# Kernel optimization log

Hardware: AMD Instinct MI355X
Metric: run time of the kernel (lower is better)

## Reference

```python
import jax, jax.numpy as jnp
import numpy as np

G = 4          # conv groups (hardcoded in module)
C = 1024       # channels (hardcoded cin=cout=1024)
SCALE = 1.0 / np.sqrt(1024.0).astype(np.float32)  # 1/sqrt(c/h), h=1


def grouped_proj(x, W, b):
    # pointwise grouped Conv1d == block-diagonal matmul over channel groups
    # x: [B, C, P], W: [G, C//G out, C//G in], b: [C]
    B, C_, P = x.shape
    xg = x.reshape(B, G, C_ // G, P)
    y = jnp.einsum('goi,bgip->bgop', W, xg)  # [B, G, C//G, P]
    return y.reshape(B, C_, P) + b[None, :, None]


def setup_inputs() -> dict:
    key = jax.random.key(0)
    ks = jax.random.split(key, 8)
    B, PK, PQ = 8, 1024, 4096
    cg = C // G
    w_std = 1.0 / np.sqrt(cg).astype(np.float32)  # ~ conv default init scale
    return {
        'Xq': jax.random.normal(ks[0], (B, C, PQ), jnp.float32),
        'Xk': jax.random.normal(ks[1], (B, C, PK), jnp.float32),
        'Wq': jax.random.normal(ks[2], (G, cg, cg), jnp.float32) * w_std,
        'bq': jax.random.normal(ks[3], (C,), jnp.float32) * 0.01,
        'Wk': jax.random.normal(ks[4], (G, cg, cg), jnp.float32) * w_std,
        'bk': jax.random.normal(ks[5], (C,), jnp.float32) * 0.01,
        'Wv': jax.random.normal(ks[6], (G, cg, cg), jnp.float32) * w_std,
        'bv': jax.random.normal(ks[7], (C,), jnp.float32) * 0.01,
    }


def reference(Xq, Xk, Wq, bq, Wk, bk, Wv, bv):
    # Q and K are both projected from Xk; V from Xq (as in the torch code)
    Q = grouped_proj(Xk, Wq, bq)   # [B, C, Pk]
    K = grouped_proj(Xk, Wk, bk)   # [B, C, Pk]
    V = grouped_proj(Xq, Wv, bv)   # [B, C, Pq]
    b, c, pk = K.shape
    pq = V.shape[-1]
    h = 1
    Qh = Q.reshape(b, h, c // h, pk)
    Kh = K.reshape(b, h, c // h, pk)
    Vh = V.reshape(b, h, c // h, pq)
    # H: [B, h, Pk, Pq], contraction over channels; softmax over dim=-2 (Pk)
    H = jnp.einsum('bhci,bhcj->bhij', Kh, Vh) * SCALE
    H = jax.nn.softmax(H, axis=-2)
    # sparse_constrain: Gram over last axis vs identity, mean squared error
    mid = jnp.einsum('bhci,bhki->bhck', H, H)          # [B, h, Pk, Pk]
    Iden = jnp.eye(pk, dtype=H.dtype)[None, None]       # broadcast over B, h
    sparse_loss = jnp.mean((mid - Iden) ** 2)
    # out: mix Q along Pk with attention H -> [B, h, C, Pq]
    out = jnp.einsum('bhij,bhki->bhkj', H, Qh).reshape(b, c, pq)
    return out, sparse_loss, H
```

## Files before the change

kernel.cpp:

```cpp
#include <hip/hip_runtime.h>

typedef _Float16 f16;
typedef f16 f16x4 __attribute__((ext_vector_type(4)));
typedef f16 f16x8 __attribute__((ext_vector_type(8)));
typedef float f32x4 __attribute__((ext_vector_type(4)));

__device__ __forceinline__ void gload16(const void* g, void* ldsbase) {
  __builtin_amdgcn_global_load_lds((const __attribute__((address_space(1))) unsigned int*)g,
                                   (__attribute__((address_space(3))) unsigned int*)ldsbase, 16, 0, 0);
}

__device__ __forceinline__ int swz(int row, int c) {
  return row * 64 + ((c ^ ((row >> 1) & 3)) << 4);
}

template<int MODE>
__global__ void __launch_bounds__(512, 2)
gemm256(const f16* __restrict__ A, const f16* __restrict__ Bm, float* __restrict__ Cf,
        f16* __restrict__ E16, f16* __restrict__ E16t,
        int K, long sA, long sB, float scale, float* __restrict__ aux) {
  __shared__ f16 sb[65536];
  const int t = threadIdx.x, l = t & 63, w = t >> 6;
  const int wr = w >> 2, wc = w & 3;
  const int bid = blockIdx.x;
  const int swzb = (bid & 7) * 64 + (bid >> 3);
  const long b = swzb >> 6;
  const int inner = swzb & 63;
  const int bx = inner >> 2, by = inner & 3;
  const char* Abyte = (const char*)(A + b * sA + (long)(by * 256) * K);
  const char* Bbyte = (const char*)(Bm + b * sB + (long)(bx * 256) * K);

  int offSrc[4];
#pragma unroll
  for (int i = 0; i < 4; ++i) {
    int cid = i * 512 + t, row = cid >> 3, slot = cid & 7;
    offSrc[i] = row * (K * 2) + ((slot ^ (row & 7)) << 4);
  }
  int offAf[8][2], offBf[4][2];
#pragma unroll
  for (int mi = 0; mi < 8; ++mi) {
    int r = wr * 128 + mi * 16 + (l & 15);
#pragma unroll
    for (int ks = 0; ks < 2; ++ks)
      offAf[mi][ks] = r * 64 + ((((ks << 2) + (l >> 4)) ^ (r & 7)) << 3);
  }
#pragma unroll
  for (int ni = 0; ni < 4; ++ni) {
    int r = wc * 64 + ni * 16 + (l & 15);
#pragma unroll
    for (int ks = 0; ks < 2; ++ks)
      offBf[ni][ks] = r * 64 + ((((ks << 2) + (l >> 4)) ^ (r & 7)) << 3);
  }

  const int NT = K >> 6;
  f32x4 acc[8][4] = {};

  auto STAGE = [&](int kt, int bsel) {
    f16* la = sb + bsel * 32768;
    f16* lb = la + 16384;
    const char* as = Abyte + (long)kt * 128;
    const char* bs = Bbyte + (long)kt * 128;
#pragma unroll
    for (int i = 0; i < 4; ++i)
      gload16(as + offSrc[i], la + (i * 512 + (w << 6)) * 8);
#pragma unroll
    for (int i = 0; i < 4; ++i)
      gload16(bs + offSrc[i], lb + (i * 512 + (w << 6)) * 8);
  };

  STAGE(0, 0);
  for (int kt = 0; kt < NT; ++kt) {
    const int cur = kt & 1;
    if (kt + 1 < NT) {
      STAGE(kt + 1, cur ^ 1);
      asm volatile("s_waitcnt vmcnt(8)" ::: "memory");
    } else {
      asm volatile("s_waitcnt vmcnt(0)" ::: "memory");
    }
    __builtin_amdgcn_s_barrier();
    asm volatile("" ::: "memory");
    const f16* la = sb + cur * 32768;
    const f16* lb = la + 16384;
#pragma unroll
    for (int ks = 0; ks < 2; ++ks) {
      f16x8 bf[4];
#pragma unroll
      for (int ni = 0; ni < 4; ++ni) bf[ni] = *(const f16x8*)(lb + offBf[ni][ks]);
#pragma unroll
      for (int mi = 0; mi < 8; ++mi) {
        f16x8 af = *(const f16x8*)(la + offAf[mi][ks]);
#pragma unroll
        for (int ni = 0; ni < 4; ++ni)
          acc[mi][ni] = __builtin_amdgcn_mfma_f32_16x16x32_f16(af, bf[ni], acc[mi][ni], 0, 0, 0);
      }
    }
    asm volatile("s_waitcnt lgkmcnt(0)" ::: "memory");
    __builtin_amdgcn_s_barrier();
    asm volatile("" ::: "memory");
  }

  const int i0 = by * 256, j0 = bx * 256;
  if (MODE == 2) {
    float csum[4] = {};
#pragma unroll
    for (int mi = 0; mi < 8; ++mi)
#pragma unroll
      for (int ni = 0; ni < 4; ++ni)
#pragma unroll
        for (int q = 0; q < 4; ++q) {
          float e = __expf(acc[mi][ni][q] * scale);
          acc[mi][ni][q] = e;
          csum[ni] += e;
        }
#pragma unroll
    for (int ni = 0; ni < 4; ++ni) {
      csum[ni] += __shfl_xor(csum[ni], 16);
      csum[ni] += __shfl_xor(csum[ni], 32);
    }
    float* colp = (float*)(sb + 34816);
    if (l < 16) {
#pragma unroll
      for (int ni = 0; ni < 4; ++ni) colp[wr * 256 + wc * 64 + ni * 16 + l] = csum[ni];
    }
    __syncthreads();
    if (t < 256) aux[(b * 4 + by) * 4096 + bx * 256 + t] = colp[t] + colp[256 + t];
    f16* E16b = E16 + b * 4194304L;
    f16* E16tb = E16t + b * 4194304L;
#pragma unroll
    for (int s = 0; s < 4; ++s) {
      if (wr == (s >> 1)) {
        const int h = s & 1;
#pragma unroll
        for (int m2 = 0; m2 < 4; ++m2)
#pragma unroll
          for (int ni = 0; ni < 4; ++ni)
#pragma unroll
            for (int q = 0; q < 4; ++q)
              sb[(m2 * 16 + (l >> 4) * 4 + q) * 264 + wc * 64 + ni * 16 + (l & 15)] =
                  (f16)acc[h * 4 + m2][ni][q];
      }
      __syncthreads();
#pragma unroll
      for (int ii = 0; ii < 4; ++ii) {
        int cid = ii * 512 + t, r = cid >> 5, cc = cid & 31;
        *(f16x8*)(E16b + (long)(i0 + s * 64 + r) * 4096 + j0 + cc * 8) =
            *(const f16x8*)(sb + r * 264 + cc * 8);
      }
      const int q4 = w >> 1, r8 = l >> 3, ic = l & 7;
#pragma unroll
      for (int ii = 0; ii < 4; ++ii) {
        int j = q4 * 64 + r8 * 8 + (w & 1) * 4 + ii;
        f16x8 v;
#pragma unroll
        for (int k2 = 0; k2 < 8; ++k2) v[k2] = sb[(ic * 8 + k2) * 264 + j];
        *(f16x8*)(E16tb + (long)(j0 + j) * 1024 + i0 + s * 64 + ic * 8) = v;
      }
      __syncthreads();
    }
  }
}

__global__ void __launch_bounds__(512, 2)
fused3(const f16* __restrict__ Q, const f16* __restrict__ Et, float* __restrict__ Cf,
       const float* __restrict__ invg,
       const f16* __restrict__ E, const f16* __restrict__ inv2sg,
       float* __restrict__ Hf, float* __restrict__ midS) {
  __shared__ f16 sb[69632];
  const int t = threadIdx.x, l = t & 63, w = t >> 6;
  const int wr = w >> 2, wc = w & 3;

  if (blockIdx.x < 160) {
    const int bid = blockIdx.x;
    const long b = bid & 7;
    const int rest = bid >> 3;
    const int h = rest & 1;
    int by = 0, r = rest >> 1;
    while (r >= 4 - by) { r -= 4 - by; ++by; }
    const int bx = by + r;
    const char* Abyte = (const char*)(E + b * 4194304L + (long)(by * 256) * 4096 + 2048L * h);
    const char* Bbyte = (const char*)(E + b * 4194304L + (long)(bx * 256) * 4096 + 2048L * h);
    const int d = bx - by;
    const int wA = (d == 1) ? 0 : (d == 2 ? 1 : -1);
    const int wB = (d == 3) ? 0 : ((d == 1 && by >= 1) ? 1 : -1);
    f16* invl = sb + 65536;
    gload16((const char*)(inv2sg + b * 4096) + (long)t * 16, invl + (w << 6) * 8);
    int offSrc[4];
#pragma unroll
    for (int i = 0; i < 4; ++i) {
      int cid = i * 512 + t, row = cid >> 3, slot = cid & 7;
      offSrc[i] = row * 8192 + ((slot ^ (row & 7)) << 4);
    }
    int offAf[8][2], offBf[4][2];
#pragma unroll
    for (int mi = 0; mi < 8; ++mi) {
      int rr = wr * 128 + mi * 16 + (l & 15);
#pragma unroll
      for (int ks = 0; ks < 2; ++ks)
        offAf[mi][ks] = rr * 64 + ((((ks << 2) + (l >> 4)) ^ (rr & 7)) << 3);
    }
#pragma unroll
    for (int ni = 0; ni < 4; ++ni) {
      int rr = wc * 64 + ni * 16 + (l & 15);
#pragma unroll
      for (int ks = 0; ks < 2; ++ks)
        offBf[ni][ks] = rr * 64 + ((((ks << 2) + (l >> 4)) ^ (rr & 7)) << 3);
    }
    f32x4 acc[8][4] = {};
    auto STAGE = [&](int lk, int bsel) {
      f16* la = sb + bsel * 32768;
      f16* lb = la + 16384;
      const char* as = Abyte + (long)lk * 128;
      const char* bs = Bbyte + (long)lk * 128;
#pragma unroll
      for (int i = 0; i < 4; ++i) gload16(as + offSrc[i], la + (i * 512 + (w << 6)) * 8);
#pragma unroll
      for (int i = 0; i < 4; ++i) gload16(bs + offSrc[i], lb + (i * 512 + (w << 6)) * 8);
    };
    STAGE(0, 0);
    for (int lk = 0; lk < 32; ++lk) {
      const int cur = lk & 1;
      if (lk + 1 < 32) {
        STAGE(lk + 1, cur ^ 1);
        const int ps = (lk - 1) >> 4;
        const bool wrote = (lk >= 1) && (wA == ps || wB == ps);
        if (wrote) asm volatile("s_waitcnt vmcnt(40)" ::: "memory");
        else       asm volatile("s_waitcnt vmcnt(8)" ::: "memory");
      } else {
        asm volatile("s_waitcnt vmcnt(0)" ::: "memory");
      }
      __builtin_amdgcn_s_barrier();
      asm volatile("" ::: "memory");
      const int ktg = 32 * h + lk;
      const f16* la = sb + cur * 32768;
      const f16* lb = la + 16384;
#pragma unroll
      for (int ks = 0; ks < 2; ++ks) {
        const f16x8 invv = *(const f16x8*)(invl + ktg * 64 + ks * 32 + ((l >> 4) << 3));
        f16x8 bf[4];
#pragma unroll
        for (int ni = 0; ni < 4; ++ni) bf[ni] = *(const f16x8*)(lb + offBf[ni][ks]);
#pragma unroll
        for (int mi = 0; mi < 8; ++mi) {
          f16x8 af = *(const f16x8*)(la + offAf[mi][ks]) * invv;
#pragma unroll
          for (int ni = 0; ni < 4; ++ni)
            acc[mi][ni] = __builtin_amdgcn_mfma_f32_16x16x32_f16(af, bf[ni], acc[mi][ni], 0, 0, 0);
        }
      }
      const int slot = lk >> 4;
      if (wA == slot || wB == slot) {
        const int panel = (wA == slot) ? by : bx;
        const f16* src = (wA == slot) ? la : lb;
        const float iv = sqrtf((float)invl[ktg * 64 + l]) * (1.0f / 64.0f);
        float* hp = Hf + b * 4194304L + (long)(panel * 256 + w * 32) * 4096 + ktg * 64 + l;
#pragma unroll
        for (int rr2 = 0; rr2 < 32; ++rr2) {
          const int row = w * 32 + rr2;
          f16 ev = src[row * 64 + ((((l >> 3) ^ (row & 7)) << 3) | (l & 7))];
          hp[(long)rr2 * 4096] = (float)ev * iv;
        }
      }
      asm volatile("s_waitcnt lgkmcnt(0)" ::: "memory");
      __builtin_amdgcn_s_barrier();
      asm volatile("" ::: "memory");
    }
    float* mt = midS + (long)(((rest >> 1) * 8 + b) * 2 + h) * 65536;
#pragma unroll
    for (int mi = 0; mi < 8; ++mi)
#pragma unroll
      for (int ni = 0; ni < 4; ++ni)
#pragma unroll
        for (int q = 0; q < 4; ++q)
          mt[(wr * 128 + mi * 16 + (l >> 4) * 4 + q) * 256 + wc * 64 + ni * 16 + (l & 15)] =
              acc[mi][ni][q];
  } else {
    const int bid = blockIdx.x - 160;
    const int swzb = (bid & 7) * 64 + (bid >> 3);
    const long b = swzb >> 6;
    const int inner = swzb & 63;
    const int bx = inner >> 2, by = inner & 3;
    const char* Abyte = (const char*)(Q + b * 1048576L + (long)(by * 256) * 1024);
    const char* Bbyte = (const char*)(Et + b * 4194304L + (long)(bx * 256) * 1024);
    int offSrc[4];
#pragma unroll
    for (int i = 0; i < 4; ++i) {
      int cid = i * 512 + t, row = cid >> 3, slot = cid & 7;
      offSrc[i] = row * 2048 + ((slot ^ (row & 7)) << 4);
    }
    int offAf[8][2], offBf[4][2];
#pragma unroll
    for (int mi = 0; mi < 8; ++mi) {
      int r = wr * 128 + mi * 16 + (l & 15);
#pragma unroll
      for (int ks = 0; ks < 2; ++ks)
        offAf[mi][ks] = r * 64 + ((((ks << 2) + (l >> 4)) ^ (r & 7)) << 3);
    }
#pragma unroll
    for (int ni = 0; ni < 4; ++ni) {
      int r = wc * 64 + ni * 16 + (l & 15);
#pragma unroll
      for (int ks = 0; ks < 2; ++ks)
        offBf[ni][ks] = r * 64 + ((((ks << 2) + (l >> 4)) ^ (r & 7)) << 3);
    }
    f32x4 acc[8][4] = {};
    auto STAGE = [&](int kt, int bsel) {
      f16* la = sb + bsel * 32768;
      f16* lb = la + 16384;
      const char* as = Abyte + (long)kt * 128;
      const char* bs = Bbyte + (long)kt * 128;
#pragma unroll
      for (int i = 0; i < 4; ++i) gload16(as + offSrc[i], la + (i * 512 + (w << 6)) * 8);
#pragma unroll
      for (int i = 0; i < 4; ++i) gload16(bs + offSrc[i], lb + (i * 512 + (w << 6)) * 8);
    };
    STAGE(0, 0);
    for (int kt = 0; kt < 16; ++kt) {
      const int cur = kt & 1;
      if (kt + 1 < 16) {
        STAGE(kt + 1, cur ^ 1);
        asm volatile("s_waitcnt vmcnt(8)" ::: "memory");
      } else {
        asm volatile("s_waitcnt vmcnt(0)" ::: "memory");
      }
      __builtin_amdgcn_s_barrier();
      asm volatile("" ::: "memory");
      const f16* la = sb + cur * 32768;
      const f16* lb = la + 16384;
#pragma unroll
      for (int ks = 0; ks < 2; ++ks) {
        f16x8 bf[4];
#pragma unroll
        for (int ni = 0; ni < 4; ++ni) bf[ni] = *(const f16x8*)(lb + offBf[ni][ks]);
#pragma unroll
        for (int mi = 0; mi < 8; ++mi) {
          f16x8 af = *(const f16x8*)(la + offAf[mi][ks]);
#pragma unroll
          for (int ni = 0; ni < 4; ++ni)
            acc[mi][ni] = __builtin_amdgcn_mfma_f32_16x16x32_f16(af, bf[ni], acc[mi][ni], 0, 0, 0);
        }
      }
      asm volatile("s_waitcnt lgkmcnt(0)" ::: "memory");
      __builtin_amdgcn_s_barrier();
      asm volatile("" ::: "memory");
    }
    const float* ip = invg + b * 4096 + bx * 256 + wc * 64;
    float iv[4];
#pragma unroll
    for (int ni = 0; ni < 4; ++ni) iv[ni] = ip[ni * 16 + (l & 15)];
    float* Cb = Cf + b * 4194304L + (long)(by * 256 + wr * 128) * 4096 + bx * 256 + wc * 64;
#pragma unroll
    for (int mi = 0; mi < 8; ++mi)
#pragma unroll
      for (int ni = 0; ni < 4; ++ni)
#pragma unroll
        for (int q = 0; q < 4; ++q)
          Cb[(long)(mi * 16 + (l >> 4) * 4 + q) * 4096 + ni * 16 + (l & 15)] = acc[mi][ni][q] * iv[ni];
  }
}

__global__ void __launch_bounds__(256)
gram_red(const float* __restrict__ midS, float* __restrict__ parts) {
  const int tile = blockIdx.x, ck = blockIdx.y, t = threadIdx.x;
  int by = 0, r = tile >> 3;
  while (r >= 4 - by) { r -= 4 - by; ++by; }
  const int bx = by + r;
  const bool diag = (by == bx);
  const float* m0 = midS + (long)(tile * 2) * 65536 + ck * 8192;
  const float* m1 = m0 + 65536;
  float p = 0.f;
  for (int i = t; i < 8192; i += 256) {
    int gi = ck * 8192 + i;
    float e = (m0[i] + m1[i]) * (1.0f / 4096.0f);
    if (diag && (gi >> 8) == (gi & 255)) e -= 1.f;
    p += e * e;
  }
  if (!diag) p *= 2.f;
#pragma unroll
  for (int d2 = 32; d2; d2 >>= 1) p += __shfl_down(p, d2);
  __shared__ float red[4];
  if ((t & 63) == 0) red[t >> 6] = p;
  __syncthreads();
  if (t == 0) parts[tile * 8 + ck] = red[0] + red[1] + red[2] + red[3];
}

__global__ void __launch_bounds__(512)
proj_all(const float* __restrict__ Xk, const float* __restrict__ Xq,
         const f16* __restrict__ Wq16, const f16* __restrict__ Wk16, const f16* __restrict__ Wv16,
         const float* __restrict__ bq, const float* __restrict__ bk, const float* __restrict__ bv,
         f16* __restrict__ Q, f16* __restrict__ Kt, f16* __restrict__ Vt) {
  __shared__ f16 sb[20480];
  const int t = threadIdx.x, l = t & 63, w = t >> 6;
  const int wrq = w >> 1, wcq = w & 1;

  if (blockIdx.x < 256) {
    f16* Wqs = sb;
    f16* Wks = sb + 8192;
    f16* Xs = sb + 16384;
    const int bg = blockIdx.x >> 3, g = bg & 3;
    const long b = bg >> 2;
    const int p0 = (blockIdx.x & 7) * 128;
    const float* Xb = Xk + b * 1048576 + (long)g * 262144;
    const char* WqB = (const char*)(Wq16 + g * 65536);
    const char* WkB = (const char*)(Wk16 + g * 65536);
    int wOff[2];
#pragma unroll
    for (int i = 0; i < 2; ++i) {
      int c = i * 512 + t, row = c >> 2, slot = (c & 3) ^ ((row >> 1) & 3);
      wOff[i] = row * 512 + (slot << 4);
    }
    const int xp = t & 127, xc = t >> 7;
    const float* xS = Xb + (long)(xc * 8) * 1024 + p0 + xp;
    const int xo = swz(xp, xc);
    int offW[4], offX[4];
#pragma unroll
    for (int i = 0; i < 4; ++i) {
      int rc = wrq * 64 + i * 16 + (l & 15);
      offW[i] = swz(rc, l >> 4);
      int rp = wcq * 64 + i * 16 + (l & 15);
      offX[i] = swz(rp, l >> 4);
    }
    f32x4 accq[4][4] = {}, acck[4][4] = {};
    for (int k0 = 0; k0 < 256; k0 += 32) {
#pragma unroll
      for (int i = 0; i < 2; ++i) {
        gload16(WqB + wOff[i] + k0 * 2, Wqs + (i * 512 + (w << 6)) * 8);
        gload16(WkB + wOff[i] + k0 * 2, Wks + (i * 512 + (w << 6)) * 8);
      }
      const float* xs = xS + (long)k0 * 1024;
      f16x8 v;
#pragma unroll
      for (int d = 0; d < 8; ++d) v[d] = (f16)xs[(long)d * 1024];
      *(f16x8*)((char*)Xs + xo) = v;
      __syncthreads();
      f16x8 qf[4], kf[4], xf[4];
#pragma unroll
      for (int i = 0; i < 4; ++i) {
        qf[i] = *(const f16x8*)((const char*)Wqs + offW[i]);
        kf[i] = *(const f16x8*)((const char*)Wks + offW[i]);
        xf[i] = *(const f16x8*)((const char*)Xs + offX[i]);
      }
#pragma unroll
      for (int mi = 0; mi < 4; ++mi)
#pragma unroll
        for (int ni = 0; ni < 4; ++ni) {
          accq[mi][ni] = __builtin_amdgcn_mfma_f32_16x16x32_f16(qf[mi], xf[ni], accq[mi][ni], 0, 0, 0);
          acck[ni][mi] = __builtin_amdgcn_mfma_f32_16x16x32_f16(xf[ni], kf[mi], acck[ni][mi], 0, 0, 0);
        }
      __syncthreads();
    }
    f16* Qb = Q + b * 1048576 + (long)(g * 256 + wrq * 64) * 1024 + p0 + wcq * 64;
#pragma unroll
    for (int mi = 0; mi < 4; ++mi)
#pragma unroll
      for (int q = 0; q < 4; ++q) {
        float bv2 = bq[g * 256 + wrq * 64 + mi * 16 + (l >> 4) * 4 + q];
#pragma unroll
        for (int ni = 0; ni < 4; ++ni)
          Qb[(long)(mi * 16 + (l >> 4) * 4 + q) * 1024 + ni * 16 + (l & 15)] = (f16)(accq[mi][ni][q] + bv2);
      }
    f16* Kb = Kt + b * 1048576 + (long)(p0 + wcq * 64) * 1024 + g * 256 + wrq * 64;
    float bcol[4];
#pragma unroll
    for (int ni = 0; ni < 4; ++ni) bcol[ni] = bk[g * 256 + wrq * 64 + ni * 16 + (l & 15)];
#pragma unroll
    for (int mi = 0; mi < 4; ++mi)
#pragma unroll
      for (int q = 0; q < 4; ++q)
#pragma unroll
        for (int ni = 0; ni < 4; ++ni)
          Kb[(long)(mi * 16 + (l >> 4) * 4 + q) * 1024 + ni * 16 + (l & 15)] = (f16)(acck[mi][ni][q] + bcol[ni]);
  } else {
    f16* Wvs = sb;
    f16* Xs = sb + 8192;
    const int bid2 = blockIdx.x - 256;
    const int bg = bid2 >> 5, g = bg & 3;
    const long b = bg >> 2;
    const int p0 = (bid2 & 31) * 128;
    const float* Xb = Xq + b * 4194304 + (long)g * 1048576;
    const char* WvB = (const char*)(Wv16 + g * 65536);
    int wOff[2];
#pragma unroll
    for (int i = 0; i < 2; ++i) {
      int c = i * 512 + t, row = c >> 2, slot = (c & 3) ^ ((row >> 1) & 3);
      wOff[i] = row * 512 + (slot << 4);
    }
    const int xp = t & 127, xc = t >> 7;
    const float* xS = Xb + (long)(xc * 8) * 4096 + p0 + xp;
    const int xo = swz(xp, xc);
    int offW[4], offX[4];
#pragma unroll
    for (int i = 0; i < 4; ++i) {
      int rc = wrq * 64 + i * 16 + (l & 15);
      offW[i] = swz(rc, l >> 4);
      int rp = wcq * 64 + i * 16 + (l & 15);
      offX[i] = swz(rp, l >> 4);
    }
    f32x4 acc[4][4] = {};
    for (int k0 = 0; k0 < 256; k0 += 32) {
#pragma unroll
      for (int i = 0; i < 2; ++i)
        gload16(WvB + wOff[i] + k0 * 2, Wvs + (i * 512 + (w << 6)) * 8);
      const float* xs = xS + (long)k0 * 4096;
      f16x8 v;
#pragma unroll
      for (int d = 0; d < 8; ++d) v[d] = (f16)xs[(long)d * 4096];
      *(f16x8*)((char*)Xs + xo) = v;
      __syncthreads();
      f16x8 wf[4], xf[4];
#pragma unroll
      for (int i = 0; i < 4; ++i) {
        wf[i] = *(const f16x8*)((const char*)Wvs + offW[i]);
        xf[i] = *(const f16x8*)((const char*)Xs + offX[i]);
      }
#pragma unroll
      for (int mi = 0; mi < 4; ++mi)
#pragma unroll
        for (int ni = 0; ni < 4; ++ni)
          acc[mi][ni] = __builtin_amdgcn_mfma_f32_16x16x32_f16(xf[mi], wf[ni], acc[mi][ni], 0, 0, 0);
      __syncthreads();
    }
    f16* Vb = Vt + b * 4194304 + (long)(p0 + wcq * 64) * 1024 + g * 256 + wrq * 64;
    float bcol[4];
#pragma unroll
    for (int ni = 0; ni < 4; ++ni) bcol[ni] = bv[g * 256 + wrq * 64 + ni * 16 + (l & 15)];
#pragma unroll
    for (int mi = 0; mi < 4; ++mi)
#pragma unroll
      for (int q = 0; q < 4; ++q)
#pragma unroll
        for (int ni = 0; ni < 4; ++ni)
          Vb[(long)(mi * 16 + (l >> 4) * 4 + q) * 1024 + ni * 16 + (l & 15)] = (f16)(acc[mi][ni][q] + bcol[ni]);
  }
}

__global__ void __launch_bounds__(256)
inv_k(const float* __restrict__ colsum, float* __restrict__ inv, f16* __restrict__ inv2s) {
  int gid = blockIdx.x * 256 + threadIdx.x;
  int b = gid >> 12, j = gid & 4095;
  const float* cp = colsum + (long)(b * 4) * 4096 + j;
  float s = 0.f;
#pragma unroll
  for (int my = 0; my < 4; ++my) s += cp[my * 4096];
  float iv = 1.f / s;
  inv[gid] = iv;
  inv2s[gid] = (f16)(iv * iv * 4096.0f);
}

__global__ void cvt3(const float* __restrict__ a, const float* __restrict__ b2,
                     const float* __restrict__ c, f16* __restrict__ da,
                     f16* __restrict__ db, f16* __restrict__ dc) {
  int i = blockIdx.x * 256 + threadIdx.x;
  int which = i >> 18, r = i & 262143;
  if (which == 0) da[r] = (f16)a[r];
  else if (which == 1) db[r] = (f16)b2[r];
  else dc[r] = (f16)c[r];
}

__global__ void __launch_bounds__(256)
finalize_k(const float* __restrict__ parts, float* __restrict__ o) {
  const int t = threadIdx.x;
  float s = 0.f;
  for (int i = t; i < 640; i += 256) s += parts[i];
#pragma unroll
  for (int d = 32; d; d >>= 1) s += __shfl_down(s, d);
  __shared__ float red[4];
  if ((t & 63) == 0) red[t >> 6] = s;
  __syncthreads();
  if (t == 0) *o = (red[0] + red[1] + red[2] + red[3]) * (1.0f / 8388608.0f);
}

extern "C" void kernel_launch(void* const* d_in, const int* in_sizes, int n_in,
                              void* d_out, int out_size, void* d_ws, size_t ws_size,
                              hipStream_t stream) {
  const float* Xq = (const float*)d_in[0];
  const float* Xk = (const float*)d_in[1];
  const float* Wq = (const float*)d_in[2];
  const float* bq = (const float*)d_in[3];
  const float* Wk = (const float*)d_in[4];
  const float* bk = (const float*)d_in[5];
  const float* Wv = (const float*)d_in[6];
  const float* bv = (const float*)d_in[7];
  float* out = (float*)d_out;
  float* loss_out = out + 33554432;
  float* Hf = out + 33554433;

  char* ws = (char*)d_ws;
  f16* W16q = (f16*)(ws);
  f16* W16k = (f16*)(ws + (1 << 19));
  f16* W16v = (f16*)(ws + 2L * (1 << 19));
  f16* Q16  = (f16*)(ws + 3L * (1 << 19));
  f16* Kt16 = (f16*)(ws + 3L * (1 << 19) + (1L << 24));
  f16* Vt16 = (f16*)(ws + 3L * (1 << 19) + 2L * (1 << 24));
  f16* E16  = (f16*)(ws + 3L * (1 << 19) + 2L * (1 << 24) + (1L << 26));
  f16* E16t = (f16*)(ws + 3L * (1 << 19) + 2L * (1 << 24) + 2L * (1 << 26));
  char* tail = ws + 3L * (1 << 19) + 2L * (1 << 24) + 3L * (1 << 26);
  float* parts = (float*)tail;
  float* invb  = (float*)(tail + 8192);
  f16*   inv2s = (f16*)(tail + 8192 + 131072);
  float* midS  = (float*)(tail + 8192 + 131072 + 65536);
  float* colsum = (float*)(ws);

  cvt3<<<3072, 256, 0, stream>>>(Wq, Wk, Wv, W16q, W16k, W16v);

  proj_all<<<1280, 512, 0, stream>>>(Xk, Xq, W16q, W16k, W16v, bq, bk, bv, Q16, Kt16, Vt16);

  gemm256<2><<<512, 512, 0, stream>>>(Kt16, Vt16, nullptr, E16, E16t,
      1024, 1L << 20, 1L << 22, 0.03125f, colsum);

  inv_k<<<128, 256, 0, stream>>>(colsum, invb, inv2s);

  fused3<<<672, 512, 0, stream>>>(Q16, E16t, out, invb, E16, inv2s, Hf, midS);

  gram_red<<<dim3(80, 8), 256, 0, stream>>>(midS, parts);
  finalize_k<<<1, 256, 0, stream>>>(parts, loss_out);
}
```

Before: 375.7 us.

## Fold Gram-loss reduction and finalize into fused3 via atomic counters

Removes the separate gram_red and finalize_k launches by appending 80 extra blocks to fused3. These blocks spin on a global counter until all 160 Gram-tile blocks have written midS, then each reduces one tile. A second counter lets the last block sum the partials into the loss. Counters are zeroed in cvt3. This saves two launches and lets the reduction overlap the out-GEMM blocks, but the extra blocks busy-wait and depend on the Gram blocks being scheduled first to avoid stalls.

```diff
diff --git a/kernel.cpp b/kernel.cpp
--- a/kernel.cpp
+++ b/kernel.cpp
@@ -164,7 +164,9 @@
 fused3(const f16* __restrict__ Q, const f16* __restrict__ Et, float* __restrict__ Cf,
        const float* __restrict__ invg,
        const f16* __restrict__ E, const f16* __restrict__ inv2sg,
-       float* __restrict__ Hf, float* __restrict__ midS) {
+       float* __restrict__ Hf, float* __restrict__ midS,
+       float* __restrict__ parts, int* __restrict__ ctrG, int* __restrict__ ctrR,
+       float* __restrict__ loss_out) {
   __shared__ f16 sb[69632];
   const int t = threadIdx.x, l = t & 63, w = t >> 6;
   const int wr = w >> 2, wc = w & 3;
@@ -273,7 +275,10 @@
         for (int q = 0; q < 4; ++q)
           mt[(wr * 128 + mi * 16 + (l >> 4) * 4 + q) * 256 + wc * 64 + ni * 16 + (l & 15)] =
               acc[mi][ni][q];
-  } else {
+    __threadfence();
+    __syncthreads();
+    if (t == 0) atomicAdd(ctrG, 1);
+  } else if (blockIdx.x < 672) {
     const int bid = blockIdx.x - 160;
     const int swzb = (bid & 7) * 64 + (bid >> 3);
     const long b = swzb >> 6;
@@ -355,32 +360,46 @@
 #pragma unroll
         for (int q = 0; q < 4; ++q)
           Cb[(long)(mi * 16 + (l >> 4) * 4 + q) * 4096 + ni * 16 + (l & 15)] = acc[mi][ni][q] * iv[ni];
+  } else {
+    const int tile = blockIdx.x - 672;
+    if (t == 0) {
+      while (atomicAdd(ctrG, 0) < 160) __builtin_amdgcn_s_sleep(16);
+    }
+    __syncthreads();
+    __threadfence();
+    int by = 0, r = tile >> 3;
+    while (r >= 4 - by) { r -= 4 - by; ++by; }
+    const int bx = by + r;
+    const bool diag = (by == bx);
+    const float* m0 = midS + (long)(tile * 2) * 65536;
+    const float* m1 = m0 + 65536;
+    float p = 0.f;
+    for (int i = t; i < 65536; i += 512) {
+      float e = (m0[i] + m1[i]) * (1.0f / 4096.0f);
+      if (diag && (i >> 8) == (i & 255)) e -= 1.f;
+      p += e * e;
+    }
+    if (!diag) p *= 2.f;
+#pragma unroll
+    for (int d2 = 32; d2; d2 >>= 1) p += __shfl_down(p, d2);
+    __shared__ float red[8];
+    if (l == 0) red[w] = p;
+    __syncthreads();
+    if (t == 0) {
+      float s = 0.f;
+#pragma unroll
+      for (int i = 0; i < 8; ++i) s += red[i];
+      parts[tile] = s;
+      __threadfence();
+      int old = atomicAdd(ctrR, 1);
+      if (old == 79) {
+        __threadfence();
+        float tot = 0.f;
+        for (int i = 0; i < 80; ++i) tot += parts[i];
+        *loss_out = tot * (1.0f / 8388608.0f);
+      }
+    }
   }
-}
-
-__global__ void __launch_bounds__(256)
-gram_red(const float* __restrict__ midS, float* __restrict__ parts) {
-  const int tile = blockIdx.x, ck = blockIdx.y, t = threadIdx.x;
-  int by = 0, r = tile >> 3;
-  while (r >= 4 - by) { r -= 4 - by; ++by; }
-  const int bx = by + r;
-  const bool diag = (by == bx);
-  const float* m0 = midS + (long)(tile * 2) * 65536 + ck * 8192;
-  const float* m1 = m0 + 65536;
-  float p = 0.f;
-  for (int i = t; i < 8192; i += 256) {
-    int gi = ck * 8192 + i;
-    float e = (m0[i] + m1[i]) * (1.0f / 4096.0f);
-    if (diag && (gi >> 8) == (gi & 255)) e -= 1.f;
-    p += e * e;
-  }
-  if (!diag) p *= 2.f;
-#pragma unroll
-  for (int d2 = 32; d2; d2 >>= 1) p += __shfl_down(p, d2);
-  __shared__ float red[4];
-  if ((t & 63) == 0) red[t >> 6] = p;
-  __syncthreads();
-  if (t == 0) parts[tile * 8 + ck] = red[0] + red[1] + red[2] + red[3];
 }
 
 __global__ void __launch_bounds__(512)
@@ -548,25 +567,13 @@
 
 __global__ void cvt3(const float* __restrict__ a, const float* __restrict__ b2,
                      const float* __restrict__ c, f16* __restrict__ da,
-                     f16* __restrict__ db, f16* __restrict__ dc) {
+                     f16* __restrict__ db, f16* __restrict__ dc, int* __restrict__ ctrs) {
   int i = blockIdx.x * 256 + threadIdx.x;
+  if (i < 2) ctrs[i] = 0;
   int which = i >> 18, r = i & 262143;
   if (which == 0) da[r] = (f16)a[r];
   else if (which == 1) db[r] = (f16)b2[r];
   else dc[r] = (f16)c[r];
-}
-
-__global__ void __launch_bounds__(256)
-finalize_k(const float* __restrict__ parts, float* __restrict__ o) {
-  const int t = threadIdx.x;
-  float s = 0.f;
-  for (int i = t; i < 640; i += 256) s += parts[i];
-#pragma unroll
-  for (int d = 32; d; d >>= 1) s += __shfl_down(s, d);
-  __shared__ float red[4];
-  if ((t & 63) == 0) red[t >> 6] = s;
-  __syncthreads();
-  if (t == 0) *o = (red[0] + red[1] + red[2] + red[3]) * (1.0f / 8388608.0f);
 }
 
 extern "C" void kernel_launch(void* const* d_in, const int* in_sizes, int n_in,
@@ -595,12 +602,13 @@
   f16* E16t = (f16*)(ws + 3L * (1 << 19) + 2L * (1 << 24) + 2L * (1 << 26));
   char* tail = ws + 3L * (1 << 19) + 2L * (1 << 24) + 3L * (1 << 26);
   float* parts = (float*)tail;
+  int*   ctrs  = (int*)(tail + 4096);
   float* invb  = (float*)(tail + 8192);
   f16*   inv2s = (f16*)(tail + 8192 + 131072);
   float* midS  = (float*)(tail + 8192 + 131072 + 65536);
   float* colsum = (float*)(ws);
 
-  cvt3<<<3072, 256, 0, stream>>>(Wq, Wk, Wv, W16q, W16k, W16v);
+  cvt3<<<3072, 256, 0, stream>>>(Wq, Wk, Wv, W16q, W16k, W16v, ctrs);
 
   proj_all<<<1280, 512, 0, stream>>>(Xk, Xq, W16q, W16k, W16v, bq, bk, bv, Q16, Kt16, Vt16);
 
@@ -609,8 +617,6 @@
 
   inv_k<<<128, 256, 0, stream>>>(colsum, invb, inv2s);
 
-  fused3<<<672, 512, 0, stream>>>(Q16, E16t, out, invb, E16, inv2s, Hf, midS);
-
-  gram_red<<<dim3(80, 8), 256, 0, stream>>>(midS, parts);
-  finalize_k<<<1, 256, 0, stream>>>(parts, loss_out);
-}
+  fused3<<<752, 512, 0, stream>>>(Q16, E16t, out, invb, E16, inv2s, Hf, midS,
+                                  parts, ctrs, ctrs + 1, loss_out);
+}
```

Result: slower. 511.7 us (+36.2%).
